# Kernel tuning notes

Hardware: AMD Instinct MI355X
Metric: run time of the kernel (lower is better)

Reference implementation:

```python
import jax, jax.numpy as jnp
import numpy as np

B, T, E, H, V, L = 16, 512, 1024, 512, 10000, 64
A, CCH, K = 256, 10, 101  # attention dim, location-conv channels, conv kernel width


def setup_inputs() -> dict:
    key = jax.random.key(0)
    ks = jax.random.split(key, 16)
    n = lambda i, shape: jax.random.normal(ks[i], shape, jnp.float32) * 0.02
    return {
        'hbatch': jax.random.normal(ks[0], (B, T, E), jnp.float32),
        'lengths': jax.random.randint(ks[1], (B,), T // 2, T + 1),
        'targets': jax.random.randint(ks[2], (B, L), 0, V),
        # decoder weights (stored (in, out); math identical to torch Linear)
        'W_sy': n(3, (H, H)),
        'W_gy': n(4, (E, H)), 'b_gy': jnp.zeros((H,), jnp.float32),
        'W_yy': n(5, (H, V)), 'b_yy': jnp.zeros((V,), jnp.float32),
        'E_ys': n(6, (V, 4 * H)),
        'W_ss': n(7, (H, 4 * H)),
        'W_gs': n(8, (E, 4 * H)), 'b_gs': jnp.zeros((4 * H,), jnp.float32),
        # location-aware additive attention params
        'W_se': n(9, (H, A)), 'W_he': n(10, (E, A)), 'W_fe': n(11, (CCH, A)),
        'b_att': jnp.zeros((A,), jnp.float32), 'w_att': n(12, (A,)),
        'F_conv': n(13, (CCH, 1, K)),
    }


def reference(hbatch, lengths, targets, W_sy, W_gy, b_gy, W_yy, b_yy, E_ys,
              W_ss, W_gs, b_gs, W_se, W_he, W_fe, b_att, w_att, F_conv):
    Bn, Tn, En = hbatch.shape
    Hn = W_sy.shape[0]
    mask = jnp.arange(Tn)[None, :] < lengths[:, None]          # (B, T) valid-frame mask
    enc_proj = jnp.einsum('bte,ea->bta', hbatch, W_he)          # (B, T, A), step-invariant

    def attend(s, alpha):
        # location features: conv over previous attention weights (B,1,T)->(B,CCH,T)
        conv = jax.lax.conv_general_dilated(
            alpha, F_conv, (1,), 'SAME',
            dimension_numbers=('NCH', 'OIH', 'NCH'))
        f_proj = jnp.einsum('bct,ca->bta', conv, W_fe)          # (B, T, A)
        e = jnp.tanh(enc_proj + f_proj + (s @ W_se)[:, None, :] + b_att) @ w_att  # (B, T)
        e = jnp.where(mask, e, -1e30)
        a = jax.nn.softmax(e, axis=1)                           # masked softmax over frames
        g = jnp.einsum('bt,bte->be', a, hbatch)                 # context (B, E)
        return g, a[:, None, :]

    def step(carry, tgt):
        s, c, alpha = carry
        g, alpha = attend(s, alpha)
        y = jnp.tanh(g @ W_gy + b_gy + s @ W_sy) @ W_yy + b_yy  # (B, V)
        rec = E_ys[tgt] + s @ W_ss + g @ W_gs + b_gs            # (B, 4H)
        i, f, cg, o = jnp.split(rec, 4, axis=1)
        c = jax.nn.sigmoid(f) * c + jax.nn.sigmoid(i) * jnp.tanh(cg)
        s = jax.nn.sigmoid(o) * jnp.tanh(c)
        return (s, c, alpha), y

    init = (jnp.zeros((Bn, Hn), hbatch.dtype),
            jnp.zeros((Bn, Hn), hbatch.dtype),
            jnp.zeros((Bn, 1, Tn), hbatch.dtype))
    _, ys = jax.lax.scan(step, init, targets.T)                 # ys: (L, B, V)
    return ys.transpose(1, 0, 2)                                # youtput: (B, L, V)
```

## Files before the change

kernel.cpp:

```cpp
#include <hip/hip_runtime.h>
#include <cmath>

#define B_ 16
#define T_ 512
#define E_ 1024
#define H_ 512
#define V_ 10000
#define L_ 64
#define A_ 256
#define CC_ 10
#define K_ 101
#define H4_ 2048

__device__ __forceinline__ float sigm(float x) { return 1.f / (1.f + expf(-x)); }

__global__ __launch_bounds__(256) void p0_init(float* alpha, float* s, float* g,
                                               float* c0, float* swse,
                                               const float* __restrict__ b_att) {
    int i = blockIdx.x * 256 + threadIdx.x;
    if (i < B_ * T_) alpha[i] = 0.f;
    if (i < B_ * H_) { s[i] = 0.f; c0[i] = 0.f; }
    if (i < B_ * E_) g[i] = 0.f;
    if (i < B_ * A_) swse[i] = b_att[i & (A_ - 1)];
}

__global__ __launch_bounds__(256) void p1_encproj(const float* __restrict__ hb,
                                                  const float* __restrict__ W_he,
                                                  float* __restrict__ ep) {
    __shared__ float As[16][68];
    __shared__ float Bs[16][68];
    const int tid = threadIdx.x;
    const int row0 = blockIdx.x * 64;
    const int n0 = blockIdx.y * 64;
    const int tn = tid & 15, tm = tid >> 4;
    float acc[4][4] = {};
    for (int k0 = 0; k0 < E_; k0 += 16) {
        {
            int m = tid >> 2, kq = (tid & 3) * 4;
            float4 v = *(const float4*)(hb + (size_t)(row0 + m) * E_ + k0 + kq);
            As[kq + 0][m] = v.x; As[kq + 1][m] = v.y;
            As[kq + 2][m] = v.z; As[kq + 3][m] = v.w;
        }
        {
            int kk = tid & 15, nq = (tid >> 4) * 4;
            float4 v = *(const float4*)(W_he + (size_t)(k0 + kk) * A_ + n0 + nq);
            *(float4*)&Bs[kk][nq] = v;
        }
        __syncthreads();
        #pragma unroll
        for (int kk = 0; kk < 16; ++kk) {
            float4 av = *(const float4*)&As[kk][tm * 4];
            float4 bv = *(const float4*)&Bs[kk][tn * 4];
            acc[0][0] += av.x * bv.x; acc[0][1] += av.x * bv.y; acc[0][2] += av.x * bv.z; acc[0][3] += av.x * bv.w;
            acc[1][0] += av.y * bv.x; acc[1][1] += av.y * bv.y; acc[1][2] += av.y * bv.z; acc[1][3] += av.y * bv.w;
            acc[2][0] += av.z * bv.x; acc[2][1] += av.z * bv.y; acc[2][2] += av.z * bv.z; acc[2][3] += av.z * bv.w;
            acc[3][0] += av.w * bv.x; acc[3][1] += av.w * bv.y; acc[3][2] += av.w * bv.z; acc[3][3] += av.w * bv.w;
        }
        __syncthreads();
    }
    #pragma unroll
    for (int i = 0; i < 4; ++i) {
        float4 o = make_float4(acc[i][0], acc[i][1], acc[i][2], acc[i][3]);
        *(float4*)(ep + (size_t)(row0 + tm * 4 + i) * A_ + n0 + tn * 4) = o;
    }
}

__global__ __launch_bounds__(256) void k1_scores(const float* __restrict__ swse_g,
                                                 const float* __restrict__ alpha,
                                                 float* __restrict__ e_out,
                                                 const float* __restrict__ enc_proj,
                                                 const float* __restrict__ w_att,
                                                 const float* __restrict__ F_conv,
                                                 const float* __restrict__ W_fe,
                                                 const int* __restrict__ lengths) {
    const int tt = blockIdx.x, b = blockIdx.y, tid = threadIdx.x;
    const int t0 = tt * 32;
    __shared__ float wfe[CC_ * A_];
    __shared__ float watt[A_];
    __shared__ float swse[A_];
    __shared__ float ash[132];
    __shared__ float conv[CC_][32];
    for (int i = tid; i < CC_ * A_; i += 256) wfe[i] = W_fe[i];
    if (tid < A_) { watt[tid] = w_att[tid]; swse[tid] = swse_g[b * A_ + tid]; }
    if (tid < 132) {
        int t = t0 - 50 + tid;
        ash[tid] = (t >= 0 && t < T_) ? alpha[b * T_ + t] : 0.f;
    }
    __syncthreads();
    {
        int t = tid & 31, cb = tid >> 5;
        for (int c = cb; c < CC_; c += 8) {
            const float* Fc = F_conv + c * K_;
            float acc = 0.f;
            #pragma unroll 4
            for (int k = 0; k < K_; ++k) acc += ash[t + k] * Fc[k];
            conv[c][t] = acc;
        }
    }
    __syncthreads();
    const int wv = tid >> 6, lane = tid & 63;
    const int len = lengths[b];
    for (int i = 0; i < 8; ++i) {
        int tl = wv * 8 + i, t = t0 + tl;
        float cv[CC_];
        #pragma unroll
        for (int c = 0; c < CC_; ++c) cv[c] = conv[c][tl];
        const float* ep = enc_proj + ((size_t)(b * T_ + t)) * A_;
        float v = 0.f;
        #pragma unroll
        for (int j = 0; j < 4; ++j) {
            int a = lane + j * 64;
            float z = ep[a] + swse[a];
            #pragma unroll
            for (int c = 0; c < CC_; ++c) z += cv[c] * wfe[c * A_ + a];
            v += tanhf(z) * watt[a];
        }
        #pragma unroll
        for (int off = 32; off; off >>= 1) v += __shfl_xor(v, off);
        if (lane == 0) e_out[b * T_ + t] = (t < len) ? v : -1e30f;
    }
}

__global__ __launch_bounds__(256) void k3_softmax_g(const float* __restrict__ e_in,
                                                    float* __restrict__ alpha,
                                                    const float* __restrict__ hbatch,
                                                    float* __restrict__ g) {
    const int tt = blockIdx.x, b = blockIdx.y, tid = threadIdx.x;
    __shared__ float red[8];
    __shared__ float a_sh[32];
    float e0 = e_in[b * T_ + tid];
    float e1 = e_in[b * T_ + 256 + tid];
    float m = fmaxf(e0, e1);
    #pragma unroll
    for (int off = 32; off; off >>= 1) m = fmaxf(m, __shfl_xor(m, off));
    if ((tid & 63) == 0) red[tid >> 6] = m;
    __syncthreads();
    m = fmaxf(fmaxf(red[0], red[1]), fmaxf(red[2], red[3]));
    float z = expf(e0 - m) + expf(e1 - m);
    #pragma unroll
    for (int off = 32; off; off >>= 1) z += __shfl_xor(z, off);
    if ((tid & 63) == 0) red[4 + (tid >> 6)] = z;
    __syncthreads();
    z = (red[4] + red[5]) + (red[6] + red[7]);
    float invz = 1.f / z;
    if (tt == 0) {
        alpha[b * T_ + tid] = expf(e0 - m) * invz;
        alpha[b * T_ + 256 + tid] = expf(e1 - m) * invz;
    }
    if (tid < 32) a_sh[tid] = expf(e_in[b * T_ + tt * 32 + tid] - m) * invz;
    __syncthreads();
    float4 acc = make_float4(0.f, 0.f, 0.f, 0.f);
    const float4* hb = (const float4*)(hbatch + ((size_t)(b * T_ + tt * 32)) * E_);
    #pragma unroll 4
    for (int j = 0; j < 32; ++j) {
        float av = a_sh[j];
        float4 hv = hb[j * (E_ / 4) + tid];
        acc.x += av * hv.x; acc.y += av * hv.y; acc.z += av * hv.z; acc.w += av * hv.w;
    }
    float* gp = g + b * E_ + tid * 4;
    atomicAdd(gp + 0, acc.x); atomicAdd(gp + 1, acc.y);
    atomicAdd(gp + 2, acc.z); atomicAdd(gp + 3, acc.w);
}

__global__ __launch_bounds__(256) void k4a_uv(const float* __restrict__ g,
                                              const float* __restrict__ s,
                                              const float* __restrict__ W_gy,
                                              const float* __restrict__ W_sy,
                                              const float* __restrict__ W_gs,
                                              const float* __restrict__ W_ss,
                                              float* __restrict__ uv) {
    const int tid = threadIdx.x;
    const int col_loc = tid & 15, b = tid >> 4;
    const int col = blockIdx.x * 16 + col_loc;
    const float* Wg; const float* Ws; int ld, cw;
    if (blockIdx.x < 32) { Wg = W_gy; Ws = W_sy; ld = H_; cw = col; }
    else                 { Wg = W_gs; Ws = W_ss; ld = H4_; cw = col - H_; }
    float acc = 0.f;
    const float4* g4 = (const float4*)(g + b * E_);
    #pragma unroll 2
    for (int kq = 0; kq < E_ / 4; ++kq) {
        float4 iv = g4[kq];
        int k = kq * 4;
        acc += iv.x * Wg[(size_t)(k + 0) * ld + cw];
        acc += iv.y * Wg[(size_t)(k + 1) * ld + cw];
        acc += iv.z * Wg[(size_t)(k + 2) * ld + cw];
        acc += iv.w * Wg[(size_t)(k + 3) * ld + cw];
    }
    const float4* s4 = (const float4*)(s + b * H_);
    #pragma unroll 2
    for (int kq = 0; kq < H_ / 4; ++kq) {
        float4 iv = s4[kq];
        int k = kq * 4;
        acc += iv.x * Ws[(size_t)(k + 0) * ld + cw];
        acc += iv.y * Ws[(size_t)(k + 1) * ld + cw];
        acc += iv.z * Ws[(size_t)(k + 2) * ld + cw];
        acc += iv.w * Ws[(size_t)(k + 3) * ld + cw];
    }
    uv[col * 16 + b] = acc;
}

__global__ __launch_bounds__(256) void k5_y_state(int l,
    const float* __restrict__ uv, const float* __restrict__ b_gy,
    const float* __restrict__ W_yy, const float* __restrict__ b_yy,
    float* __restrict__ out,
    const float* __restrict__ E_ys, const float* __restrict__ b_gs,
    const int* __restrict__ targets,
    const float* __restrict__ c_prev, float* __restrict__ c_cur,
    float* __restrict__ s_glob, float* __restrict__ swse,
    float* __restrict__ g,
    const float* __restrict__ W_se, const float* __restrict__ b_att) {
    __shared__ float lds[2 * 16 * 512];
    const int tid = threadIdx.x;
    const int bx = blockIdx.x;
    if (bx < V_ / 16) {
        float* u_lds = lds;
        float* w_lds = lds + 16 * 512;
        const int v0 = bx * 16;
        for (int i = tid; i < 8192; i += 256) {
            int h = i >> 4, bb = i & 15;
            int xr = (bb & 7) << 2;
            u_lds[bb * 512 + (h ^ xr)] = tanhf(uv[i] + b_gy[h]);
            w_lds[bb * 512 + (h ^ xr)] = W_yy[(size_t)h * V_ + v0 + bb];
        }
        __syncthreads();
        const int vl = tid & 15, b = tid >> 4;
        const int xu = (b & 7) << 2, xw = (vl & 7) << 2;
        const float* up = u_lds + b * 512;
        const float* wp = w_lds + vl * 512;
        float ax = 0.f, ay = 0.f, az = 0.f, aw = 0.f;
        #pragma unroll 8
        for (int h = 0; h < H_; h += 4) {
            float4 u4 = *(const float4*)(up + (h ^ xu));
            float4 w4 = *(const float4*)(wp + (h ^ xw));
            ax += u4.x * w4.x; ay += u4.y * w4.y;
            az += u4.z * w4.z; aw += u4.w * w4.w;
        }
        float acc = (ax + ay) + (az + aw);
        int v = v0 + vl;
        out[((size_t)b * L_ + l) * V_ + v] = acc + b_yy[v];
    } else {
        float* s_lds = lds;
        const int aq = bx - V_ / 16;
        for (int j = tid; j < B_ * H_; j += 256) {
            int b = j >> 9, h = j & 511;
            int tgt = targets[b * L_ + l];
            const float* ey = E_ys + (size_t)tgt * H4_;
            float iv = uv[(512 + h) * 16 + b] + ey[h] + b_gs[h];
            float fv = uv[(512 + h + 512) * 16 + b] + ey[h + 512] + b_gs[h + 512];
            float cg = uv[(512 + h + 1024) * 16 + b] + ey[h + 1024] + b_gs[h + 1024];
            float ov = uv[(512 + h + 1536) * 16 + b] + ey[h + 1536] + b_gs[h + 1536];
            float cn = sigm(fv) * c_prev[j] + sigm(iv) * tanhf(cg);
            float sn = sigm(ov) * tanhf(cn);
            s_lds[j] = sn;
            if (aq == 0) { c_cur[j] = cn; s_glob[j] = sn; }
        }
        __syncthreads();
        const int a_loc = tid & 63, bq = tid >> 6;
        const int a = aq * 64 + a_loc;
        float acc0 = b_att[a], acc1 = b_att[a], acc2 = b_att[a], acc3 = b_att[a];
        #pragma unroll 4
        for (int h = 0; h < H_; ++h) {
            float w = W_se[h * A_ + a];
            acc0 += w * s_lds[(bq + 0) * 512 + h];
            acc1 += w * s_lds[(bq + 4) * 512 + h];
            acc2 += w * s_lds[(bq + 8) * 512 + h];
            acc3 += w * s_lds[(bq + 12) * 512 + h];
        }
        swse[(bq + 0) * A_ + a] = acc0;
        swse[(bq + 4) * A_ + a] = acc1;
        swse[(bq + 8) * A_ + a] = acc2;
        swse[(bq + 12) * A_ + a] = acc3;
        if (aq == 0) for (int i = tid; i < B_ * E_; i += 256) g[i] = 0.f;
    }
}

extern "C" void kernel_launch(void* const* d_in, const int* in_sizes, int n_in,
                              void* d_out, int out_size, void* d_ws, size_t ws_size,
                              hipStream_t stream) {
    (void)in_sizes; (void)n_in; (void)out_size; (void)ws_size;
    const float* hbatch = (const float*)d_in[0];
    const int* lengths  = (const int*)d_in[1];
    const int* targets  = (const int*)d_in[2];
    const float* W_sy   = (const float*)d_in[3];
    const float* W_gy   = (const float*)d_in[4];
    const float* b_gy   = (const float*)d_in[5];
    const float* W_yy   = (const float*)d_in[6];
    const float* b_yy   = (const float*)d_in[7];
    const float* E_ys   = (const float*)d_in[8];
    const float* W_ss   = (const float*)d_in[9];
    const float* W_gs   = (const float*)d_in[10];
    const float* b_gs   = (const float*)d_in[11];
    const float* W_se   = (const float*)d_in[12];
    const float* W_he   = (const float*)d_in[13];
    const float* W_fe   = (const float*)d_in[14];
    const float* b_att  = (const float*)d_in[15];
    const float* w_att  = (const float*)d_in[16];
    const float* F_conv = (const float*)d_in[17];
    float* out = (float*)d_out;

    float* ws = (float*)d_ws;
    float* enc_proj = ws;
    float* alpha    = enc_proj + 2097152;
    float* e_buf    = alpha + 8192;
    float* g        = e_buf + 8192;
    float* s        = g + 16384;
    float* c0       = s + 8192;
    float* c1       = c0 + 8192;
    float* swse     = c1 + 8192;
    float* uv       = swse + 4096;

    p0_init<<<dim3(64), dim3(256), 0, stream>>>(alpha, s, g, c0, swse, b_att);
    p1_encproj<<<dim3(128, 4), dim3(256), 0, stream>>>(hbatch, W_he, enc_proj);

    for (int l = 0; l < L_; ++l) {
        float* c_prev = (l & 1) ? c1 : c0;
        float* c_cur  = (l & 1) ? c0 : c1;
        k1_scores<<<dim3(16, 16), dim3(256), 0, stream>>>(
            swse, alpha, e_buf, enc_proj, w_att, F_conv, W_fe, lengths);
        k3_softmax_g<<<dim3(16, 16), dim3(256), 0, stream>>>(
            e_buf, alpha, hbatch, g);
        k4a_uv<<<dim3(160), dim3(256), 0, stream>>>(
            g, s, W_gy, W_sy, W_gs, W_ss, uv);
        k5_y_state<<<dim3(V_ / 16 + 4), dim3(256), 0, stream>>>(
            l, uv, b_gy, W_yy, b_yy, out,
            E_ys, b_gs, targets, c_prev, c_cur, s, swse, g, W_se, b_att);
    }
}
```

Before: 13.63 ms.

## Fuse whole decoder into one persistent kernel with grid barriers

Replaces the per-step launches (four kernels times 64 steps plus setup) with a single persistent kernel of 256 blocks. Phases are separated by a software grid barrier built on atomics. Work is also repartitioned: the conv is split across k-chunks, the context is computed per E-chunk without atomics, and split-K partial sums with tile counters are used. The output projection is restructured and fast exp/tanh approximations replace tanhf and expf. This removes launch overhead, but the code depends on all 256 blocks being co-resident and the spin barrier can time out silently.

Result: faster. 12.11 ms (-11.2%).

```diff
diff --git a/kernel.cpp b/kernel.cpp
--- a/kernel.cpp
+++ b/kernel.cpp
@@ -11,266 +11,367 @@
 #define CC_ 10
 #define K_ 101
 #define H4_ 2048
-
-__device__ __forceinline__ float sigm(float x) { return 1.f / (1.f + expf(-x)); }
-
-__global__ __launch_bounds__(256) void p0_init(float* alpha, float* s, float* g,
-                                               float* c0, float* swse,
-                                               const float* __restrict__ b_att) {
-    int i = blockIdx.x * 256 + threadIdx.x;
-    if (i < B_ * T_) alpha[i] = 0.f;
-    if (i < B_ * H_) { s[i] = 0.f; c0[i] = 0.f; }
-    if (i < B_ * E_) g[i] = 0.f;
-    if (i < B_ * A_) swse[i] = b_att[i & (A_ - 1)];
-}
-
-__global__ __launch_bounds__(256) void p1_encproj(const float* __restrict__ hb,
-                                                  const float* __restrict__ W_he,
-                                                  float* __restrict__ ep) {
-    __shared__ float As[16][68];
-    __shared__ float Bs[16][68];
-    const int tid = threadIdx.x;
-    const int row0 = blockIdx.x * 64;
-    const int n0 = blockIdx.y * 64;
-    const int tn = tid & 15, tm = tid >> 4;
-    float acc[4][4] = {};
-    for (int k0 = 0; k0 < E_; k0 += 16) {
-        {
-            int m = tid >> 2, kq = (tid & 3) * 4;
-            float4 v = *(const float4*)(hb + (size_t)(row0 + m) * E_ + k0 + kq);
-            As[kq + 0][m] = v.x; As[kq + 1][m] = v.y;
-            As[kq + 2][m] = v.z; As[kq + 3][m] = v.w;
-        }
-        {
-            int kk = tid & 15, nq = (tid >> 4) * 4;
-            float4 v = *(const float4*)(W_he + (size_t)(k0 + kk) * A_ + n0 + nq);
-            *(float4*)&Bs[kk][nq] = v;
-        }
-        __syncthreads();
-        #pragma unroll
-        for (int kk = 0; kk < 16; ++kk) {
-            float4 av = *(const float4*)&As[kk][tm * 4];
-            float4 bv = *(const float4*)&Bs[kk][tn * 4];
-            acc[0][0] += av.x * bv.x; acc[0][1] += av.x * bv.y; acc[0][2] += av.x * bv.z; acc[0][3] += av.x * bv.w;
-            acc[1][0] += av.y * bv.x; acc[1][1] += av.y * bv.y; acc[1][2] += av.y * bv.z; acc[1][3] += av.y * bv.w;
-            acc[2][0] += av.z * bv.x; acc[2][1] += av.z * bv.y; acc[2][2] += av.z * bv.z; acc[2][3] += av.z * bv.w;
-            acc[3][0] += av.w * bv.x; acc[3][1] += av.w * bv.y; acc[3][2] += av.w * bv.z; acc[3][3] += av.w * bv.w;
-        }
-        __syncthreads();
-    }
-    #pragma unroll
-    for (int i = 0; i < 4; ++i) {
-        float4 o = make_float4(acc[i][0], acc[i][1], acc[i][2], acc[i][3]);
-        *(float4*)(ep + (size_t)(row0 + tm * 4 + i) * A_ + n0 + tn * 4) = o;
-    }
-}
-
-__global__ __launch_bounds__(256) void k1_scores(const float* __restrict__ swse_g,
-                                                 const float* __restrict__ alpha,
-                                                 float* __restrict__ e_out,
-                                                 const float* __restrict__ enc_proj,
-                                                 const float* __restrict__ w_att,
-                                                 const float* __restrict__ F_conv,
-                                                 const float* __restrict__ W_fe,
-                                                 const int* __restrict__ lengths) {
-    const int tt = blockIdx.x, b = blockIdx.y, tid = threadIdx.x;
-    const int t0 = tt * 32;
-    __shared__ float wfe[CC_ * A_];
-    __shared__ float watt[A_];
-    __shared__ float swse[A_];
-    __shared__ float ash[132];
-    __shared__ float conv[CC_][32];
-    for (int i = tid; i < CC_ * A_; i += 256) wfe[i] = W_fe[i];
-    if (tid < A_) { watt[tid] = w_att[tid]; swse[tid] = swse_g[b * A_ + tid]; }
-    if (tid < 132) {
-        int t = t0 - 50 + tid;
-        ash[tid] = (t >= 0 && t < T_) ? alpha[b * T_ + t] : 0.f;
+#define NBLK 256
+#define NTHR 256
+
+struct Params {
+    const float* hbatch; const int* lengths; const int* targets;
+    const float *W_sy, *W_gy, *b_gy, *W_yy, *b_yy, *E_ys, *W_ss, *W_gs, *b_gs;
+    const float *W_se, *W_he, *W_fe, *b_att, *w_att, *F_conv;
+    float* out;
+    float *enc_proj, *alpha, *e, *g, *s, *c0, *c1, *swse, *u_pre, *rec_pre, *u_t;
+    int *tilecnt, *bar;
+};
+
+__device__ __forceinline__ float fsigm(float x) {
+    return 1.f / (1.f + __expf(-x));
+}
+__device__ __forceinline__ float ftanh(float x) {
+    float ax = fabsf(x);
+    float ex = __expf(-2.f * ax);
+    float t = (1.f - ex) / (1.f + ex);
+    return copysignf(t, x);
+}
+
+__global__ void bar_init(int* tilecnt_and_bar) {
+    if (threadIdx.x < 128) tilecnt_and_bar[threadIdx.x] = 0;
+}
+
+__device__ __forceinline__ void gsync(int* bar, int target) {
+    __syncthreads();
+    if (threadIdx.x == 0) {
+        int arrived = __hip_atomic_fetch_add(&bar[0], 1, __ATOMIC_ACQ_REL,
+                                             __HIP_MEMORY_SCOPE_AGENT);
+        if (arrived == NBLK - 1) {
+            __hip_atomic_store(&bar[0], 0, __ATOMIC_RELAXED, __HIP_MEMORY_SCOPE_AGENT);
+            __hip_atomic_store(&bar[32], target, __ATOMIC_RELEASE, __HIP_MEMORY_SCOPE_AGENT);
+        } else {
+            int spins = 0;
+            while (__hip_atomic_load(&bar[32], __ATOMIC_ACQUIRE,
+                                     __HIP_MEMORY_SCOPE_AGENT) < target) {
+                __builtin_amdgcn_s_sleep(2);
+                if (++spins > (1 << 26)) break;
+            }
+        }
     }
     __syncthreads();
+}
+
+__global__ __launch_bounds__(NTHR, 1) void mega(Params p) {
+    const int bx = blockIdx.x, tid = threadIdx.x;
+    const int lane = tid & 63, wv = tid >> 6;
+    __shared__ __align__(16) float s_res[3840];
+    __shared__ __align__(16) float s_scr[10560];
+    int bt = 0;
+
+    for (int i = tid; i < CC_ * A_; i += NTHR) s_res[i] = p.W_fe[i];
+    if (tid < A_) s_res[2560 + tid] = p.w_att[tid];
+    for (int i = tid; i < CC_ * K_; i += NTHR) s_res[2816 + i] = p.F_conv[i];
+
+    if (bx < B_) {
+        p.alpha[bx * T_ + tid] = 0.f; p.alpha[bx * T_ + 256 + tid] = 0.f;
+        p.s[bx * H_ + tid] = 0.f;     p.s[bx * H_ + 256 + tid] = 0.f;
+        p.c0[bx * H_ + tid] = 0.f;    p.c0[bx * H_ + 256 + tid] = 0.f;
+        p.swse[bx * A_ + tid] = p.b_att[tid];
+    }
+
     {
-        int t = tid & 31, cb = tid >> 5;
-        for (int c = cb; c < CC_; c += 8) {
-            const float* Fc = F_conv + c * K_;
-            float acc = 0.f;
+        float* As = s_scr;
+        float* Bs = s_scr + 1088;
+        for (int tt2 = 0; tt2 < 2; ++tt2) {
+            const int tile = bx * 2 + tt2;
+            const int row0 = (tile >> 2) * 64, n0 = (tile & 3) * 64;
+            const int tn = tid & 15, tm = tid >> 4;
+            float acc[4][4] = {};
+            for (int k0 = 0; k0 < E_; k0 += 16) {
+                __syncthreads();
+                {
+                    int m = tid >> 2, kq = (tid & 3) * 4;
+                    float4 v = *(const float4*)(p.hbatch + (size_t)(row0 + m) * E_ + k0 + kq);
+                    As[(kq + 0) * 68 + m] = v.x; As[(kq + 1) * 68 + m] = v.y;
+                    As[(kq + 2) * 68 + m] = v.z; As[(kq + 3) * 68 + m] = v.w;
+                }
+                {
+                    int kk = tid & 15, nq = (tid >> 4) * 4;
+                    float4 v = *(const float4*)(p.W_he + (size_t)(k0 + kk) * A_ + n0 + nq);
+                    *(float4*)&Bs[kk * 68 + nq] = v;
+                }
+                __syncthreads();
+                #pragma unroll
+                for (int kk = 0; kk < 16; ++kk) {
+                    float4 av = *(const float4*)&As[kk * 68 + tm * 4];
+                    float4 bv = *(const float4*)&Bs[kk * 68 + tn * 4];
+                    acc[0][0] += av.x * bv.x; acc[0][1] += av.x * bv.y; acc[0][2] += av.x * bv.z; acc[0][3] += av.x * bv.w;
+                    acc[1][0] += av.y * bv.x; acc[1][1] += av.y * bv.y; acc[1][2] += av.y * bv.z; acc[1][3] += av.y * bv.w;
+                    acc[2][0] += av.z * bv.x; acc[2][1] += av.z * bv.y; acc[2][2] += av.z * bv.z; acc[2][3] += av.z * bv.w;
+                    acc[3][0] += av.w * bv.x; acc[3][1] += av.w * bv.y; acc[3][2] += av.w * bv.z; acc[3][3] += av.w * bv.w;
+                }
+            }
+            #pragma unroll
+            for (int i = 0; i < 4; ++i) {
+                float4 o = make_float4(acc[i][0], acc[i][1], acc[i][2], acc[i][3]);
+                *(float4*)(p.enc_proj + (size_t)(row0 + tm * 4 + i) * A_ + n0 + tn * 4) = o;
+            }
+        }
+    }
+
+    gsync(p.bar, ++bt);
+
+    for (int l = 0; l < L_; ++l) {
+        {
+            const int b = bx >> 4, tc = bx & 15, t0 = tc * 32;
+            float* ash   = s_scr;
+            float* conv  = s_scr + 132;
+            float* cpart = s_scr + 708;
+            if (tid < 132) {
+                int t = t0 - 50 + tid;
+                ash[tid] = (t >= 0 && t < T_) ? p.alpha[b * T_ + t] : 0.f;
+            }
+            __syncthreads();
+            {
+                const int t = tid & 31, kq = tid >> 5;
+                const int kbeg = kq * 13, kend = (kbeg + 13 < K_) ? kbeg + 13 : K_;
+                float accc[CC_] = {};
+                for (int k = kbeg; k < kend; ++k) {
+                    float av = ash[t + k];
+                    #pragma unroll
+                    for (int c = 0; c < CC_; ++c) accc[c] += av * s_res[2816 + c * K_ + k];
+                }
+                #pragma unroll
+                for (int c = 0; c < CC_; ++c) cpart[(c * 8 + kq) * 32 + t] = accc[c];
+            }
+            __syncthreads();
+            for (int i = tid; i < CC_ * 32; i += NTHR) {
+                int c = i >> 5, t = i & 31;
+                float sv = 0.f;
+                #pragma unroll
+                for (int q = 0; q < 8; ++q) sv += cpart[(c * 8 + q) * 32 + t];
+                conv[c * 32 + t] = sv;
+            }
+            __syncthreads();
+            float wfeR[4][CC_], swl4[4], watt4[4];
+            #pragma unroll
+            for (int j = 0; j < 4; ++j) {
+                int a = lane + j * 64;
+                swl4[j] = p.swse[b * A_ + a];
+                watt4[j] = s_res[2560 + a];
+                #pragma unroll
+                for (int c = 0; c < CC_; ++c) wfeR[j][c] = s_res[c * A_ + a];
+            }
+            const int len = p.lengths[b];
+            for (int i = 0; i < 8; ++i) {
+                int tl = wv * 8 + i, t = t0 + tl;
+                float cvv[CC_];
+                #pragma unroll
+                for (int c = 0; c < CC_; ++c) cvv[c] = conv[c * 32 + tl];
+                const float* ep = p.enc_proj + (size_t)(b * T_ + t) * A_;
+                float v = 0.f;
+                #pragma unroll
+                for (int j = 0; j < 4; ++j) {
+                    int a = lane + j * 64;
+                    float z = ep[a] + swl4[j];
+                    #pragma unroll
+                    for (int c = 0; c < CC_; ++c) z += cvv[c] * wfeR[j][c];
+                    v += ftanh(z) * watt4[j];
+                }
+                #pragma unroll
+                for (int off = 32; off; off >>= 1) v += __shfl_xor(v, off);
+                if (lane == 0) p.e[b * T_ + t] = (t < len) ? v : -1e30f;
+            }
+        }
+        gsync(p.bar, ++bt);
+
+        {
+            const int b = bx >> 4, ec = bx & 15;
+            float* a_sh = s_scr;
+            float* red  = s_scr + 512;
+            float* pg   = s_scr + 528;
+            float v0 = p.e[b * T_ + tid], v1 = p.e[b * T_ + 256 + tid];
+            float m = fmaxf(v0, v1);
+            #pragma unroll
+            for (int off = 32; off; off >>= 1) m = fmaxf(m, __shfl_xor(m, off));
+            if ((tid & 63) == 0) red[tid >> 6] = m;
+            __syncthreads();
+            m = fmaxf(fmaxf(red[0], red[1]), fmaxf(red[2], red[3]));
+            float z0 = __expf(v0 - m), z1 = __expf(v1 - m);
+            float z = z0 + z1;
+            #pragma unroll
+            for (int off = 32; off; off >>= 1) z += __shfl_xor(z, off);
+            if ((tid & 63) == 0) red[8 + (tid >> 6)] = z;
+            __syncthreads();
+            z = (red[8] + red[9]) + (red[10] + red[11]);
+            float invz = 1.f / z;
+            float a0 = z0 * invz, a1 = z1 * invz;
+            a_sh[tid] = a0; a_sh[256 + tid] = a1;
+            if (ec == 0) {
+                p.alpha[b * T_ + tid] = a0; p.alpha[b * T_ + 256 + tid] = a1;
+            }
+            __syncthreads();
+            const int e4 = tid & 15, tq = tid >> 4;
+            float4 acc = make_float4(0.f, 0.f, 0.f, 0.f);
+            const float* hb = p.hbatch + (size_t)(b * T_ + tq * 32) * E_ + ec * 64 + e4 * 4;
             #pragma unroll 4
-            for (int k = 0; k < K_; ++k) acc += ash[t + k] * Fc[k];
-            conv[c][t] = acc;
-        }
-    }
-    __syncthreads();
-    const int wv = tid >> 6, lane = tid & 63;
-    const int len = lengths[b];
-    for (int i = 0; i < 8; ++i) {
-        int tl = wv * 8 + i, t = t0 + tl;
-        float cv[CC_];
-        #pragma unroll
-        for (int c = 0; c < CC_; ++c) cv[c] = conv[c][tl];
-        const float* ep = enc_proj + ((size_t)(b * T_ + t)) * A_;
-        float v = 0.f;
-        #pragma unroll
-        for (int j = 0; j < 4; ++j) {
-            int a = lane + j * 64;
-            float z = ep[a] + swse[a];
-            #pragma unroll
-            for (int c = 0; c < CC_; ++c) z += cv[c] * wfe[c * A_ + a];
-            v += tanhf(z) * watt[a];
-        }
-        #pragma unroll
-        for (int off = 32; off; off >>= 1) v += __shfl_xor(v, off);
-        if (lane == 0) e_out[b * T_ + t] = (t < len) ? v : -1e30f;
-    }
-}
-
-__global__ __launch_bounds__(256) void k3_softmax_g(const float* __restrict__ e_in,
-                                                    float* __restrict__ alpha,
-                                                    const float* __restrict__ hbatch,
-                                                    float* __restrict__ g) {
-    const int tt = blockIdx.x, b = blockIdx.y, tid = threadIdx.x;
-    __shared__ float red[8];
-    __shared__ float a_sh[32];
-    float e0 = e_in[b * T_ + tid];
-    float e1 = e_in[b * T_ + 256 + tid];
-    float m = fmaxf(e0, e1);
-    #pragma unroll
-    for (int off = 32; off; off >>= 1) m = fmaxf(m, __shfl_xor(m, off));
-    if ((tid & 63) == 0) red[tid >> 6] = m;
-    __syncthreads();
-    m = fmaxf(fmaxf(red[0], red[1]), fmaxf(red[2], red[3]));
-    float z = expf(e0 - m) + expf(e1 - m);
-    #pragma unroll
-    for (int off = 32; off; off >>= 1) z += __shfl_xor(z, off);
-    if ((tid & 63) == 0) red[4 + (tid >> 6)] = z;
-    __syncthreads();
-    z = (red[4] + red[5]) + (red[6] + red[7]);
-    float invz = 1.f / z;
-    if (tt == 0) {
-        alpha[b * T_ + tid] = expf(e0 - m) * invz;
-        alpha[b * T_ + 256 + tid] = expf(e1 - m) * invz;
-    }
-    if (tid < 32) a_sh[tid] = expf(e_in[b * T_ + tt * 32 + tid] - m) * invz;
-    __syncthreads();
-    float4 acc = make_float4(0.f, 0.f, 0.f, 0.f);
-    const float4* hb = (const float4*)(hbatch + ((size_t)(b * T_ + tt * 32)) * E_);
-    #pragma unroll 4
-    for (int j = 0; j < 32; ++j) {
-        float av = a_sh[j];
-        float4 hv = hb[j * (E_ / 4) + tid];
-        acc.x += av * hv.x; acc.y += av * hv.y; acc.z += av * hv.z; acc.w += av * hv.w;
-    }
-    float* gp = g + b * E_ + tid * 4;
-    atomicAdd(gp + 0, acc.x); atomicAdd(gp + 1, acc.y);
-    atomicAdd(gp + 2, acc.z); atomicAdd(gp + 3, acc.w);
-}
-
-__global__ __launch_bounds__(256) void k4a_uv(const float* __restrict__ g,
-                                              const float* __restrict__ s,
-                                              const float* __restrict__ W_gy,
-                                              const float* __restrict__ W_sy,
-                                              const float* __restrict__ W_gs,
-                                              const float* __restrict__ W_ss,
-                                              float* __restrict__ uv) {
-    const int tid = threadIdx.x;
-    const int col_loc = tid & 15, b = tid >> 4;
-    const int col = blockIdx.x * 16 + col_loc;
-    const float* Wg; const float* Ws; int ld, cw;
-    if (blockIdx.x < 32) { Wg = W_gy; Ws = W_sy; ld = H_; cw = col; }
-    else                 { Wg = W_gs; Ws = W_ss; ld = H4_; cw = col - H_; }
-    float acc = 0.f;
-    const float4* g4 = (const float4*)(g + b * E_);
-    #pragma unroll 2
-    for (int kq = 0; kq < E_ / 4; ++kq) {
-        float4 iv = g4[kq];
-        int k = kq * 4;
-        acc += iv.x * Wg[(size_t)(k + 0) * ld + cw];
-        acc += iv.y * Wg[(size_t)(k + 1) * ld + cw];
-        acc += iv.z * Wg[(size_t)(k + 2) * ld + cw];
-        acc += iv.w * Wg[(size_t)(k + 3) * ld + cw];
-    }
-    const float4* s4 = (const float4*)(s + b * H_);
-    #pragma unroll 2
-    for (int kq = 0; kq < H_ / 4; ++kq) {
-        float4 iv = s4[kq];
-        int k = kq * 4;
-        acc += iv.x * Ws[(size_t)(k + 0) * ld + cw];
-        acc += iv.y * Ws[(size_t)(k + 1) * ld + cw];
-        acc += iv.z * Ws[(size_t)(k + 2) * ld + cw];
-        acc += iv.w * Ws[(size_t)(k + 3) * ld + cw];
-    }
-    uv[col * 16 + b] = acc;
-}
-
-__global__ __launch_bounds__(256) void k5_y_state(int l,
-    const float* __restrict__ uv, const float* __restrict__ b_gy,
-    const float* __restrict__ W_yy, const float* __restrict__ b_yy,
-    float* __restrict__ out,
-    const float* __restrict__ E_ys, const float* __restrict__ b_gs,
-    const int* __restrict__ targets,
-    const float* __restrict__ c_prev, float* __restrict__ c_cur,
-    float* __restrict__ s_glob, float* __restrict__ swse,
-    float* __restrict__ g,
-    const float* __restrict__ W_se, const float* __restrict__ b_att) {
-    __shared__ float lds[2 * 16 * 512];
-    const int tid = threadIdx.x;
-    const int bx = blockIdx.x;
-    if (bx < V_ / 16) {
-        float* u_lds = lds;
-        float* w_lds = lds + 16 * 512;
-        const int v0 = bx * 16;
-        for (int i = tid; i < 8192; i += 256) {
-            int h = i >> 4, bb = i & 15;
-            int xr = (bb & 7) << 2;
-            u_lds[bb * 512 + (h ^ xr)] = tanhf(uv[i] + b_gy[h]);
-            w_lds[bb * 512 + (h ^ xr)] = W_yy[(size_t)h * V_ + v0 + bb];
-        }
-        __syncthreads();
-        const int vl = tid & 15, b = tid >> 4;
-        const int xu = (b & 7) << 2, xw = (vl & 7) << 2;
-        const float* up = u_lds + b * 512;
-        const float* wp = w_lds + vl * 512;
-        float ax = 0.f, ay = 0.f, az = 0.f, aw = 0.f;
-        #pragma unroll 8
-        for (int h = 0; h < H_; h += 4) {
-            float4 u4 = *(const float4*)(up + (h ^ xu));
-            float4 w4 = *(const float4*)(wp + (h ^ xw));
-            ax += u4.x * w4.x; ay += u4.y * w4.y;
-            az += u4.z * w4.z; aw += u4.w * w4.w;
-        }
-        float acc = (ax + ay) + (az + aw);
-        int v = v0 + vl;
-        out[((size_t)b * L_ + l) * V_ + v] = acc + b_yy[v];
-    } else {
-        float* s_lds = lds;
-        const int aq = bx - V_ / 16;
-        for (int j = tid; j < B_ * H_; j += 256) {
-            int b = j >> 9, h = j & 511;
-            int tgt = targets[b * L_ + l];
-            const float* ey = E_ys + (size_t)tgt * H4_;
-            float iv = uv[(512 + h) * 16 + b] + ey[h] + b_gs[h];
-            float fv = uv[(512 + h + 512) * 16 + b] + ey[h + 512] + b_gs[h + 512];
-            float cg = uv[(512 + h + 1024) * 16 + b] + ey[h + 1024] + b_gs[h + 1024];
-            float ov = uv[(512 + h + 1536) * 16 + b] + ey[h + 1536] + b_gs[h + 1536];
-            float cn = sigm(fv) * c_prev[j] + sigm(iv) * tanhf(cg);
-            float sn = sigm(ov) * tanhf(cn);
-            s_lds[j] = sn;
-            if (aq == 0) { c_cur[j] = cn; s_glob[j] = sn; }
-        }
-        __syncthreads();
-        const int a_loc = tid & 63, bq = tid >> 6;
-        const int a = aq * 64 + a_loc;
-        float acc0 = b_att[a], acc1 = b_att[a], acc2 = b_att[a], acc3 = b_att[a];
-        #pragma unroll 4
-        for (int h = 0; h < H_; ++h) {
-            float w = W_se[h * A_ + a];
-            acc0 += w * s_lds[(bq + 0) * 512 + h];
-            acc1 += w * s_lds[(bq + 4) * 512 + h];
-            acc2 += w * s_lds[(bq + 8) * 512 + h];
-            acc3 += w * s_lds[(bq + 12) * 512 + h];
-        }
-        swse[(bq + 0) * A_ + a] = acc0;
-        swse[(bq + 4) * A_ + a] = acc1;
-        swse[(bq + 8) * A_ + a] = acc2;
-        swse[(bq + 12) * A_ + a] = acc3;
-        if (aq == 0) for (int i = tid; i < B_ * E_; i += 256) g[i] = 0.f;
+            for (int tt = 0; tt < 32; ++tt) {
+                float av = a_sh[tq * 32 + tt];
+                float4 hv = *(const float4*)(hb + (size_t)tt * E_);
+                acc.x += av * hv.x; acc.y += av * hv.y;
+                acc.z += av * hv.z; acc.w += av * hv.w;
+            }
+            *(float4*)(pg + tid * 4) = acc;
+            __syncthreads();
+            if (tid < 64) {
+                float sv = 0.f;
+                #pragma unroll
+                for (int q = 0; q < 16; ++q) sv += pg[(q * 16 + (tid >> 2)) * 4 + (tid & 3)];
+                p.g[b * E_ + ec * 64 + tid] = sv;
+            }
+            int idx = bx * NTHR + tid;
+            if (idx < 8192) p.u_pre[idx] = 0.f;
+            else if (idx < 40960) p.rec_pre[idx - 8192] = 0.f;
+            if (bx == NBLK - 1 && tid < 8) p.tilecnt[tid] = 0;
+        }
+        gsync(p.bar, ++bt);
+
+        if (bx < 240) {
+            const int ct = bx / 6, kc = bx % 6;
+            const int c0 = ct * 64, k0 = kc * 256;
+            float* xs = s_scr;
+            for (int i = tid; i < 1024; i += NTHR) {
+                int b = i >> 6, off = (i & 63) * 4;
+                const float* src = (k0 < E_) ? (p.g + (size_t)b * E_ + k0 + off)
+                                             : (p.s + (size_t)b * H_ + (k0 - E_) + off);
+                *(float4*)&xs[b * 256 + off] = *(const float4*)src;
+            }
+            __syncthreads();
+            const float* Wb; int ld, cc;
+            if (ct < 8) {
+                ld = H_; cc = c0 + lane;
+                Wb = (k0 < E_) ? (p.W_gy + (size_t)k0 * H_) : (p.W_sy + (size_t)(k0 - E_) * H_);
+            } else {
+                ld = H4_; cc = c0 - 512 + lane;
+                Wb = (k0 < E_) ? (p.W_gs + (size_t)k0 * H4_) : (p.W_ss + (size_t)(k0 - E_) * H4_);
+            }
+            Wb += cc;
+            const int b0 = wv * 4;
+            const float* x0 = xs + (b0 + 0) * 256;
+            const float* x1 = xs + (b0 + 1) * 256;
+            const float* x2 = xs + (b0 + 2) * 256;
+            const float* x3 = xs + (b0 + 3) * 256;
+            float a0 = 0.f, a1 = 0.f, a2 = 0.f, a3 = 0.f;
+            #pragma unroll 4
+            for (int k = 0; k < 256; k += 4) {
+                float w0 = Wb[(size_t)(k + 0) * ld];
+                float w1 = Wb[(size_t)(k + 1) * ld];
+                float w2 = Wb[(size_t)(k + 2) * ld];
+                float w3 = Wb[(size_t)(k + 3) * ld];
+                float4 v0 = *(const float4*)(x0 + k);
+                float4 v1 = *(const float4*)(x1 + k);
+                float4 v2 = *(const float4*)(x2 + k);
+                float4 v3 = *(const float4*)(x3 + k);
+                a0 += w0 * v0.x + w1 * v0.y + w2 * v0.z + w3 * v0.w;
+                a1 += w0 * v1.x + w1 * v1.y + w2 * v1.z + w3 * v1.w;
+                a2 += w0 * v2.x + w1 * v2.y + w2 * v2.z + w3 * v2.w;
+                a3 += w0 * v3.x + w1 * v3.y + w2 * v3.z + w3 * v3.w;
+            }
+            if (ct < 8) {
+                atomicAdd(p.u_pre + (size_t)(b0 + 0) * H_ + cc, a0);
+                atomicAdd(p.u_pre + (size_t)(b0 + 1) * H_ + cc, a1);
+                atomicAdd(p.u_pre + (size_t)(b0 + 2) * H_ + cc, a2);
+                atomicAdd(p.u_pre + (size_t)(b0 + 3) * H_ + cc, a3);
+                __threadfence();
+                __syncthreads();
+                int* lflag = (int*)&s_scr[4096];
+                if (tid == 0) {
+                    int done = __hip_atomic_fetch_add(&p.tilecnt[ct], 1, __ATOMIC_ACQ_REL,
+                                                      __HIP_MEMORY_SCOPE_AGENT);
+                    lflag[0] = (done == 5) ? 1 : 0;
+                }
+                __syncthreads();
+                if (lflag[0]) {
+                    #pragma unroll
+                    for (int bi = 0; bi < 4; ++bi) {
+                        int b = b0 + bi;
+                        float v = __hip_atomic_load(p.u_pre + (size_t)b * H_ + cc,
+                                                    __ATOMIC_RELAXED, __HIP_MEMORY_SCOPE_AGENT);
+                        p.u_t[(size_t)b * H_ + cc] = ftanh(v + p.b_gy[cc]);
+                    }
+                }
+            } else {
+                atomicAdd(p.rec_pre + (size_t)(b0 + 0) * H4_ + cc, a0);
+                atomicAdd(p.rec_pre + (size_t)(b0 + 1) * H4_ + cc, a1);
+                atomicAdd(p.rec_pre + (size_t)(b0 + 2) * H4_ + cc, a2);
+                atomicAdd(p.rec_pre + (size_t)(b0 + 3) * H4_ + cc, a3);
+            }
+        }
+        gsync(p.bar, ++bt);
+
+        if (bx < 157) {
+            float* u_sh = s_scr;
+            for (int i = tid; i < 2048; i += NTHR)
+                ((float4*)u_sh)[i] = ((const float4*)p.u_t)[i];
+            __syncthreads();
+            const int v = bx * 64 + lane;
+            const int vc = (v < V_) ? v : V_ - 1;
+            const int b0 = wv * 4;
+            float acc[4] = {0.f, 0.f, 0.f, 0.f};
+            #pragma unroll 2
+            for (int k0 = 0; k0 < H_; k0 += 8) {
+                float w[8];
+                #pragma unroll
+                for (int kk = 0; kk < 8; ++kk)
+                    w[kk] = p.W_yy[(size_t)(k0 + kk) * V_ + vc];
+                #pragma unroll
+                for (int bi = 0; bi < 4; ++bi) {
+                    const float* ub = u_sh + (b0 + bi) * H_ + k0;
+                    float4 ua = *(const float4*)ub;
+                    float4 ub4 = *(const float4*)(ub + 4);
+                    acc[bi] += ua.x * w[0] + ua.y * w[1] + ua.z * w[2] + ua.w * w[3]
+                             + ub4.x * w[4] + ub4.y * w[5] + ub4.z * w[6] + ub4.w * w[7];
+                }
+            }
+            if (v < V_) {
+                float by = p.b_yy[v];
+                #pragma unroll
+                for (int bi = 0; bi < 4; ++bi)
+                    p.out[((size_t)(b0 + bi) * L_ + l) * V_ + v] = acc[bi] + by;
+            }
+        } else if (bx < 221) {
+            const int j2 = bx - 157, b = j2 & 15, q = j2 >> 4;
+            float* s_sh = s_scr;
+            float* pr   = s_scr + 512;
+            const int tgt = p.targets[b * L_ + l];
+            const float* ey = p.E_ys + (size_t)tgt * H4_;
+            const float* rc = p.rec_pre + (size_t)b * H4_;
+            const float* cprev = ((l & 1) ? p.c1 : p.c0) + b * H_;
+            float* ccur = ((l & 1) ? p.c0 : p.c1) + b * H_;
+            for (int h = tid; h < H_; h += NTHR) {
+                float iv  = rc[h]        + ey[h]        + p.b_gs[h];
+                float fv  = rc[512 + h]  + ey[512 + h]  + p.b_gs[512 + h];
+                float cg2 = rc[1024 + h] + ey[1024 + h] + p.b_gs[1024 + h];
+                float ov  = rc[1536 + h] + ey[1536 + h] + p.b_gs[1536 + h];
+                float cn = fsigm(fv) * cprev[h] + fsigm(iv) * ftanh(cg2);
+                float sn = fsigm(ov) * ftanh(cn);
+                s_sh[h] = sn;
+                if (q == 0) { ccur[h] = cn; p.s[b * H_ + h] = sn; }
+            }
+            __syncthreads();
+            const int al = tid & 63, hq = tid >> 6;
+            const int a = q * 64 + al;
+            float fa = 0.f;
+            #pragma unroll 4
+            for (int hh = 0; hh < 128; ++hh) {
+                int h = hq * 128 + hh;
+                fa += s_sh[h] * p.W_se[(size_t)h * A_ + a];
+            }
+            pr[hq * 64 + al] = fa;
+            __syncthreads();
+            if (tid < 64) {
+                float sv = pr[tid] + pr[64 + tid] + pr[128 + tid] + pr[192 + tid]
+                         + p.b_att[q * 64 + tid];
+                p.swse[b * A_ + q * 64 + tid] = sv;
+            }
+        }
+        gsync(p.bar, ++bt);
     }
 }
 
@@ -278,51 +379,42 @@
                               void* d_out, int out_size, void* d_ws, size_t ws_size,
                               hipStream_t stream) {
     (void)in_sizes; (void)n_in; (void)out_size; (void)ws_size;
-    const float* hbatch = (const float*)d_in[0];
-    const int* lengths  = (const int*)d_in[1];
-    const int* targets  = (const int*)d_in[2];
-    const float* W_sy   = (const float*)d_in[3];
-    const float* W_gy   = (const float*)d_in[4];
-    const float* b_gy   = (const float*)d_in[5];
-    const float* W_yy   = (const float*)d_in[6];
-    const float* b_yy   = (const float*)d_in[7];
-    const float* E_ys   = (const float*)d_in[8];
-    const float* W_ss   = (const float*)d_in[9];
-    const float* W_gs   = (const float*)d_in[10];
-    const float* b_gs   = (const float*)d_in[11];
-    const float* W_se   = (const float*)d_in[12];
-    const float* W_he   = (const float*)d_in[13];
-    const float* W_fe   = (const float*)d_in[14];
-    const float* b_att  = (const float*)d_in[15];
-    const float* w_att  = (const float*)d_in[16];
-    const float* F_conv = (const float*)d_in[17];
-    float* out = (float*)d_out;
+    Params p;
+    p.hbatch = (const float*)d_in[0];
+    p.lengths = (const int*)d_in[1];
+    p.targets = (const int*)d_in[2];
+    p.W_sy  = (const float*)d_in[3];
+    p.W_gy  = (const float*)d_in[4];
+    p.b_gy  = (const float*)d_in[5];
+    p.W_yy  = (const float*)d_in[6];
+    p.b_yy  = (const float*)d_in[7];
+    p.E_ys  = (const float*)d_in[8];
+    p.W_ss  = (const float*)d_in[9];
+    p.W_gs  = (const float*)d_in[10];
+    p.b_gs  = (const float*)d_in[11];
+    p.W_se  = (const float*)d_in[12];
+    p.W_he  = (const float*)d_in[13];
+    p.W_fe  = (const float*)d_in[14];
+    p.b_att = (const float*)d_in[15];
+    p.w_att = (const float*)d_in[16];
+    p.F_conv = (const float*)d_in[17];
+    p.out = (float*)d_out;
 
     float* ws = (float*)d_ws;
-    float* enc_proj = ws;
-    float* alpha    = enc_proj + 2097152;
-    float* e_buf    = alpha + 8192;
-    float* g        = e_buf + 8192;
-    float* s        = g + 16384;
-    float* c0       = s + 8192;
-    float* c1       = c0 + 8192;
-    float* swse     = c1 + 8192;
-    float* uv       = swse + 4096;
-
-    p0_init<<<dim3(64), dim3(256), 0, stream>>>(alpha, s, g, c0, swse, b_att);
-    p1_encproj<<<dim3(128, 4), dim3(256), 0, stream>>>(hbatch, W_he, enc_proj);
-
-    for (int l = 0; l < L_; ++l) {
-        float* c_prev = (l & 1) ? c1 : c0;
-        float* c_cur  = (l & 1) ? c0 : c1;
-        k1_scores<<<dim3(16, 16), dim3(256), 0, stream>>>(
-            swse, alpha, e_buf, enc_proj, w_att, F_conv, W_fe, lengths);
-        k3_softmax_g<<<dim3(16, 16), dim3(256), 0, stream>>>(
-            e_buf, alpha, hbatch, g);
-        k4a_uv<<<dim3(160), dim3(256), 0, stream>>>(
-            g, s, W_gy, W_sy, W_gs, W_ss, uv);
-        k5_y_state<<<dim3(V_ / 16 + 4), dim3(256), 0, stream>>>(
-            l, uv, b_gy, W_yy, b_yy, out,
-            E_ys, b_gs, targets, c_prev, c_cur, s, swse, g, W_se, b_att);
-    }
-}
+    p.enc_proj = ws;
+    p.alpha    = ws + 2097152;
+    p.e        = ws + 2105344;
+    p.g        = ws + 2113536;
+    p.s        = ws + 2129920;
+    p.c0       = ws + 2138112;
+    p.c1       = ws + 2146304;
+    p.swse     = ws + 2154496;
+    p.u_pre    = ws + 2158592;
+    p.rec_pre  = ws + 2166784;
+    p.u_t      = ws + 2199552;
+    p.tilecnt  = (int*)(ws + 2207744);
+    p.bar      = (int*)(ws + 2207808);
+
+    bar_init<<<dim3(1), dim3(128), 0, stream>>>(p.tilecnt);
+    mega<<<dim3(NBLK), dim3(NTHR), 0, stream>>>(p);
+}
```
